# Optimization experiments

Measured on AMD Instinct MI355X. Metric: run time of the kernel, lower is better.

## Reference

```python
import jax, jax.numpy as jnp
import numpy as np

D_MODEL = 2048
N_HEADS = 16
HEAD_DIM = D_MODEL // N_HEADS  # 128
B, T = 2, 2048


def setup_inputs() -> dict:
    key = jax.random.key(0)
    ks = jax.random.split(key, 9)
    s = 0.02
    x = jax.random.normal(ks[0], (B, T, D_MODEL), dtype=jnp.float32)
    # Per-head projection weights (stacked over heads); torch Linear y = x @ W^T + b,
    # here W is stored as [H, d_model, head_dim] so y = einsum('btc,hcd->bhtd').
    Wq = jax.random.normal(ks[1], (N_HEADS, D_MODEL, HEAD_DIM), dtype=jnp.float32) * s
    bq = jax.random.normal(ks[2], (N_HEADS, HEAD_DIM), dtype=jnp.float32) * s
    Wk = jax.random.normal(ks[3], (N_HEADS, D_MODEL, HEAD_DIM), dtype=jnp.float32) * s
    bk = jax.random.normal(ks[4], (N_HEADS, HEAD_DIM), dtype=jnp.float32) * s
    Wv = jax.random.normal(ks[5], (N_HEADS, D_MODEL, HEAD_DIM), dtype=jnp.float32) * s
    bv = jax.random.normal(ks[6], (N_HEADS, HEAD_DIM), dtype=jnp.float32) * s
    Wo = jax.random.normal(ks[7], (D_MODEL, D_MODEL), dtype=jnp.float32) * s  # used as y @ Wo
    bo = jax.random.normal(ks[8], (D_MODEL,), dtype=jnp.float32) * s
    return {"x": x, "Wq": Wq, "bq": bq, "Wk": Wk, "bk": bk,
            "Wv": Wv, "bv": bv, "Wo": Wo, "bo": bo}


def reference(x, Wq, bq, Wk, bk, Wv, bv, Wo, bo):
    # x: [B, T, C]; per-head Q/K/V projections -> [B, H, T, D]
    Bn, Tn, C = x.shape
    H, _, D = Wq.shape
    scale = D ** (-0.5)
    q = jnp.einsum('btc,hcd->bhtd', x, Wq) + bq[None, :, None, :]
    k = jnp.einsum('btc,hcd->bhtd', x, Wk) + bk[None, :, None, :]
    v = jnp.einsum('btc,hcd->bhtd', x, Wv) + bv[None, :, None, :]
    # scores [B, H, T, T] with additive causal mask (finfo.min above the diagonal)
    scores = jnp.einsum('bhtd,bhsd->bhts', q, k) * scale
    neg = jnp.finfo(scores.dtype).min
    causal = jnp.triu(jnp.full((Tn, Tn), neg, dtype=scores.dtype), k=1)
    probs = jax.nn.softmax(scores + causal, axis=-1)
    y = jnp.einsum('bhts,bhsd->bhtd', probs, v)  # [B, H, T, D]
    # concat heads along feature dim (head order preserved) then output projection
    y = y.transpose(0, 2, 1, 3).reshape(Bn, Tn, H * D)
    return y @ Wo + bo
```

## Files before the change

kernel.cpp:

```cpp
#include <hip/hip_runtime.h>
#include <stdint.h>

typedef unsigned short u16;
typedef __attribute__((ext_vector_type(4))) u16 u16x4;
typedef __attribute__((ext_vector_type(8))) u16 u16x8;
typedef __attribute__((ext_vector_type(8))) __bf16 bf16x8;
typedef __attribute__((ext_vector_type(4))) float f32x4;

#define D_MODEL 2048
#define N_HEADS 16
#define HEAD_DIM 128
#define BATCH 2
#define SEQ 2048
#define M_TOT (BATCH*SEQ)
#define N_QKV (3*D_MODEL)

__device__ __forceinline__ u16 f2b(float f) {
  union { float f; uint32_t u; } c; c.f = f;
  uint32_t u = c.u;
  uint32_t r = (u + 0x7fffu + ((u >> 16) & 1u)) >> 16;
  return (u16)r;
}

__device__ __forceinline__ void gl_lds16(const u16* g, u16* l) {
  __builtin_amdgcn_global_load_lds(
      (const __attribute__((address_space(1))) uint32_t*)g,
      (__attribute__((address_space(3))) uint32_t*)l, 16, 0, 0);
}


__global__ void cast_x_kernel(const float* __restrict__ x, u16* __restrict__ xb, int n) {
  int i = (blockIdx.x * blockDim.x + threadIdx.x) * 4;
  if (i >= n) return;
  f32x4 v = *(const f32x4*)(x + i);
  u16x4 o;
  o[0] = f2b(v[0]); o[1] = f2b(v[1]); o[2] = f2b(v[2]); o[3] = f2b(v[3]);
  *(u16x4*)(xb + i) = o;
}

__global__ void trans_wqkv_kernel(const float* __restrict__ Wq, const float* __restrict__ Wk,
                                  const float* __restrict__ Wv, u16* __restrict__ Wt) {
  __shared__ u16 Tl[128][72];
  const int hh = blockIdx.y;
  const int qkv = hh >> 4, h = hh & 15;
  const float* src = (qkv == 0 ? Wq : qkv == 1 ? Wk : Wv) + (size_t)h * 2048 * 128;
  const int k0 = blockIdx.x * 64;
  const int tid = threadIdx.x;
  for (int it = 0; it < 32; ++it) {
    int idx = it * 256 + tid;
    int k = idx >> 7, d = idx & 127;
    Tl[d][k] = f2b(src[(size_t)(k0 + k) * 128 + d]);
  }
  __syncthreads();
  for (int it = 0; it < 32; ++it) {
    int idx = it * 256 + tid;
    int d = idx >> 6, kk = idx & 63;
    Wt[(size_t)(hh * 128 + d) * 2048 + k0 + kk] = Tl[d][kk];
  }
}

__global__ void trans_wo_kernel(const float* __restrict__ Wo, u16* __restrict__ Wot) {
  __shared__ u16 Tl[128][72];
  const int k0 = blockIdx.x * 64;
  const int n0 = blockIdx.y * 128;
  const int tid = threadIdx.x;
  for (int it = 0; it < 32; ++it) {
    int idx = it * 256 + tid;
    int k = idx >> 7, n = idx & 127;
    Tl[n][k] = f2b(Wo[(size_t)(k0 + k) * 2048 + n0 + n]);
  }
  __syncthreads();
  for (int it = 0; it < 32; ++it) {
    int idx = it * 256 + tid;
    int d = idx >> 6, kk = idx & 63;
    Wot[(size_t)(n0 + d) * 2048 + k0 + kk] = Tl[d][kk];
  }
}

__global__ void transpose_v_kernel(const u16* __restrict__ vb, u16* __restrict__ vt) {
  __shared__ u16 Tl[128 * 65];
  const int bh = blockIdx.y;
  const int t0 = blockIdx.x * 64;
  const int tid = threadIdx.x;
  const u16* src = vb + (size_t)bh * 2048 * 128;
  u16* dstp = vt + (size_t)bh * 128 * 2048;
#pragma unroll
  for (int c = 0; c < 4; ++c) {
    int ci = c * 256 + tid;
    int tr = ci >> 4, d0 = (ci & 15) * 8;
    u16x8 v = *(const u16x8*)(src + (size_t)(t0 + tr) * 128 + d0);
#pragma unroll
    for (int e = 0; e < 8; ++e) Tl[(d0 + e) * 65 + tr] = v[e];
  }
  __syncthreads();
#pragma unroll
  for (int it = 0; it < 32; ++it) {
    int idx = it * 256 + tid;
    int d = idx >> 6, tt = idx & 63;
    dstp[(size_t)d * 2048 + t0 + ((tt & 15) * 4 + (tt >> 4))] = Tl[d * 65 + tt];
  }
}

template <int EPI>
__global__ __launch_bounds__(256) void gemm_kernel(
    const u16* __restrict__ A, const u16* __restrict__ B,
    u16* __restrict__ qo, u16* __restrict__ ko, u16* __restrict__ vo,
    const float* __restrict__ bq, const float* __restrict__ bk, const float* __restrict__ bv,
    float* __restrict__ outf, const float* __restrict__ bo) {
  __shared__ u16 As[128 * 32];
  __shared__ u16 Bs[128 * 32];
  constexpr int NX = (EPI == 0) ? 48 : 16;
  const int nwg = gridDim.x;
  const int q8 = nwg >> 3;
  const int bid0 = blockIdx.x;
  const int gid = (bid0 & 7) * q8 + (bid0 >> 3);
  const int m0 = (gid / NX) * 128, n0 = (gid % NX) * 128;

  const int tid = threadIdx.x;
  const int lane = tid & 63, wv = tid >> 6;
  const int wm = (wv >> 1) * 64, wn = (wv & 1) * 64;
  const int lr = lane & 15, lk = (lane >> 4) * 8;

  f32x4 zero = {0.f, 0.f, 0.f, 0.f};
  f32x4 acc[4][4];
#pragma unroll
  for (int i = 0; i < 4; ++i)
#pragma unroll
    for (int j = 0; j < 4; ++j) acc[i][j] = zero;

  const int e0 = tid * 8;
  const int row0 = e0 >> 5;
  const int col0 = e0 & 31;
  const u16* Ag = A + (size_t)(m0 + row0) * 2048 + col0;
  const u16* Bg = B + (size_t)(n0 + row0) * 2048 + col0;

  for (int kt = 0; kt < 2048; kt += 32) {
    gl_lds16(Ag + kt, As + e0);
    gl_lds16(Ag + kt + (size_t)64 * 2048, As + e0 + 64 * 32);
    gl_lds16(Bg + kt, Bs + e0);
    gl_lds16(Bg + kt + (size_t)64 * 2048, Bs + e0 + 64 * 32);
    __syncthreads();
    bf16x8 af[4], bfm[4];
#pragma unroll
    for (int i = 0; i < 4; ++i) af[i] = *(const bf16x8*)(As + (wm + i * 16 + lr) * 32 + lk);
#pragma unroll
    for (int j = 0; j < 4; ++j) bfm[j] = *(const bf16x8*)(Bs + (wn + j * 16 + lr) * 32 + lk);
#pragma unroll
    for (int i = 0; i < 4; ++i)
#pragma unroll
      for (int j = 0; j < 4; ++j)
        acc[i][j] = __builtin_amdgcn_mfma_f32_16x16x32_bf16(af[i], bfm[j], acc[i][j], 0, 0, 0);
    __syncthreads();
  }

  const int rbase = (lane >> 4) * 4;
  if (EPI == 0) {
    const int qkv = n0 >> 11, h = (n0 >> 7) & 15;
    const float* bias = (qkv == 0) ? bq : (qkv == 1) ? bk : bv;
    u16* dst = (qkv == 0) ? qo : (qkv == 1) ? ko : vo;
    const float qscale = 0.08838834764831845f * 1.4426950408889634f;
#pragma unroll
    for (int i = 0; i < 4; ++i)
#pragma unroll
      for (int j = 0; j < 4; ++j)
#pragma unroll
        for (int r = 0; r < 4; ++r) {
          int gm = m0 + wm + i * 16 + rbase + r;
          int d = wn + j * 16 + (lane & 15);
          float val = acc[i][j][r] + bias[h * 128 + d];
          if (qkv == 0) val *= qscale;
          int b = gm >> 11, t = gm & 2047;
          dst[((size_t)(b * 16 + h) * 2048 + t) * 128 + d] = f2b(val);
        }
  } else {
#pragma unroll
    for (int i = 0; i < 4; ++i)
#pragma unroll
      for (int j = 0; j < 4; ++j)
#pragma unroll
        for (int r = 0; r < 4; ++r) {
          int gm = m0 + wm + i * 16 + rbase + r;
          int gn = n0 + wn + j * 16 + (lane & 15);
          outf[(size_t)gm * 2048 + gn] = acc[i][j][r] + bo[gn];
        }
  }
}

__global__ __launch_bounds__(256) void attn_kernel(
    const u16* __restrict__ qg, const u16* __restrict__ kg,
    const u16* __restrict__ vtg, u16* __restrict__ y) {
  __shared__ u16 Kb[2][64 * 128];
  __shared__ u16 Vb[2][128 * 64];
  __shared__ u16 Pl[4][32 * 64];
  const int tid = threadIdx.x, lane = tid & 63, w = tid >> 6;
  const int bid = blockIdx.x;
  const int bh = bid & 31, qt = 15 - (bid >> 5);
  const int b = bh >> 4, h = bh & 15;
  const int lr = lane & 15, lk = (lane >> 4) * 8;
  const u16* Qp = qg + (size_t)bh * (2048 * 128);
  const u16* Kp = kg + (size_t)bh * (2048 * 128);
  const u16* Vp = vtg + (size_t)bh * (128 * 2048);

  int koff[4], voff[4], dstc[4];
#pragma unroll
  for (int c = 0; c < 4; ++c) {
    int ci = c * 256 + tid;
    dstc[c] = ci * 8;
    int kr = ci >> 4, kj = ci & 15;
    koff[c] = kr * 128 + (kj ^ (kr & 7)) * 8;
    int vd = ci >> 3, vj = ci & 7;
    voff[c] = vd * 2048 + (vj ^ (vd & 7)) * 8;
  }
  const int kxor = (lr & 7) << 4;
  const int rbase = (lane >> 4) * 4;
  const f32x4 zero = {0.f, 0.f, 0.f, 0.f};

  const int q0 = qt * 128;
  const int qw = q0 + w * 32;
  const int nt = 2 * qt + 2;

  bf16x8 qf[2][4];
#pragma unroll
  for (int s = 0; s < 2; ++s)
#pragma unroll
    for (int i = 0; i < 4; ++i)
      qf[s][i] = *(const bf16x8*)(Qp + (size_t)(qw + s * 16 + lr) * 128 + i * 32 + lk);

  f32x4 o[2][8];
#pragma unroll
  for (int s = 0; s < 2; ++s)
#pragma unroll
    for (int f = 0; f < 8; ++f) o[s][f] = zero;
  float mrow[2][4], lrow[2][4];
#pragma unroll
  for (int s = 0; s < 2; ++s)
#pragma unroll
    for (int r = 0; r < 4; ++r) { mrow[s][r] = -1e30f; lrow[s][r] = 0.f; }

#pragma unroll
  for (int c = 0; c < 4; ++c) gl_lds16(Kp + koff[c], Kb[0] + dstc[c]);
#pragma unroll
  for (int c = 0; c < 4; ++c) gl_lds16(Vp + voff[c], Vb[0] + dstc[c]);
  __syncthreads();

  int cur = 0;
  for (int t = 0; t < nt; ++t) {
    const int s0 = t * 64;
    if (t + 1 < nt) {
      const size_t skn = (size_t)(s0 + 64) * 128;
#pragma unroll
      for (int c = 0; c < 4; ++c) gl_lds16(Kp + skn + koff[c], Kb[cur ^ 1] + dstc[c]);
#pragma unroll
      for (int c = 0; c < 4; ++c) gl_lds16(Vp + (s0 + 64) + voff[c], Vb[cur ^ 1] + dstc[c]);
    }
    if (s0 <= qw + 31) {
      const char* Kc = (const char*)Kb[cur];
      f32x4 sf[2][4];
      __builtin_amdgcn_s_setprio(1);
#pragma unroll
      for (int sj = 0; sj < 4; ++sj) {
        f32x4 a0 = zero, a1 = zero;
#pragma unroll
        for (int i = 0; i < 4; ++i) {
          bf16x8 kf = *(const bf16x8*)(Kc + ((((sj * 16 + lr) * 256) + (i * 32 + lk) * 2) ^ kxor));
          a0 = __builtin_amdgcn_mfma_f32_16x16x32_bf16(qf[0][i], kf, a0, 0, 0, 0);
          a1 = __builtin_amdgcn_mfma_f32_16x16x32_bf16(qf[1][i], kf, a1, 0, 0, 0);
        }
        sf[0][sj] = a0; sf[1][sj] = a1;
      }
      __builtin_amdgcn_s_setprio(0);

      char* Pc = (char*)Pl[w];
      const bool diag = (s0 + 63 > qw);
      float pmax[2][4];
      bool need = false;
#pragma unroll
      for (int s = 0; s < 2; ++s)
#pragma unroll
        for (int r = 0; r < 4; ++r) {
          if (diag) {
            const int rq = qw + s * 16 + rbase + r;
#pragma unroll
            for (int sj = 0; sj < 4; ++sj)
              if (s0 + sj * 16 + lr > rq) sf[s][sj][r] = -1e30f;
          }
          float pm = fmaxf(fmaxf(sf[s][0][r], sf[s][1][r]),
                           fmaxf(sf[s][2][r], sf[s][3][r]));
          pmax[s][r] = pm;
          need |= (pm > mrow[s][r] + 8.f);
        }
      if (__any(need)) {
#pragma unroll
        for (int s = 0; s < 2; ++s)
#pragma unroll
          for (int r = 0; r < 4; ++r) {
            float pm = pmax[s][r];
            pm = fmaxf(pm, __shfl_xor(pm, 1));
            pm = fmaxf(pm, __shfl_xor(pm, 2));
            pm = fmaxf(pm, __shfl_xor(pm, 4));
            pm = fmaxf(pm, __shfl_xor(pm, 8));
            float mnew = fmaxf(mrow[s][r], pm);
            float sfac = __builtin_amdgcn_exp2f(mrow[s][r] - mnew);
            mrow[s][r] = mnew;
            lrow[s][r] *= sfac;
#pragma unroll
            for (int f = 0; f < 8; ++f) o[s][f][r] *= sfac;
          }
      }
#pragma unroll
      for (int s = 0; s < 2; ++s)
#pragma unroll
        for (int r = 0; r < 4; ++r) {
          const int prow = s * 16 + rbase + r;
          u16x4 pk;
          float ps = 0.f;
#pragma unroll
          for (int sj = 0; sj < 4; ++sj) {
            float p = __builtin_amdgcn_exp2f(sf[s][sj][r] - mrow[s][r]);
            ps += p;
            pk[sj] = f2b(p);
          }
          lrow[s][r] += ps;
          *(u16x4*)(Pc + ((prow * 128 + lr * 8) ^ ((prow & 7) << 4))) = pk;
        }

      const char* Vc = (const char*)Vb[cur];
      __builtin_amdgcn_s_setprio(1);
#pragma unroll
      for (int st = 0; st < 2; ++st) {
        bf16x8 pf0 = *(const bf16x8*)(Pc + (((lr * 128) + (st * 32 + lk) * 2) ^ kxor));
        bf16x8 pf1 = *(const bf16x8*)(Pc + ((((16 + lr) * 128) + (st * 32 + lk) * 2) ^ kxor));
#pragma unroll
        for (int f = 0; f < 8; ++f) {
          bf16x8 vf = *(const bf16x8*)(Vc + ((((f * 16 + lr) * 128) + (st * 32 + lk) * 2) ^ kxor));
          o[0][f] = __builtin_amdgcn_mfma_f32_16x16x32_bf16(pf0, vf, o[0][f], 0, 0, 0);
          o[1][f] = __builtin_amdgcn_mfma_f32_16x16x32_bf16(pf1, vf, o[1][f], 0, 0, 0);
        }
      }
      __builtin_amdgcn_s_setprio(0);
    }
    __syncthreads();
    cur ^= 1;
  }

#pragma unroll
  for (int s = 0; s < 2; ++s)
#pragma unroll
    for (int r = 0; r < 4; ++r) {
      float l = lrow[s][r];
      l += __shfl_xor(l, 1);
      l += __shfl_xor(l, 2);
      l += __shfl_xor(l, 4);
      l += __shfl_xor(l, 8);
      const float rinv = __builtin_amdgcn_rcpf(l);
      const int row = qw + s * 16 + rbase + r;
#pragma unroll
      for (int f = 0; f < 8; ++f)
        y[((size_t)b * 2048 + row) * 2048 + h * 128 + f * 16 + lr] =
            f2b(o[s][f][r] * rinv);
    }
}


extern "C" void kernel_launch(void* const* d_in, const int* in_sizes, int n_in,
                              void* d_out, int out_size, void* d_ws, size_t ws_size,
                              hipStream_t stream) {
  const float* x  = (const float*)d_in[0];
  const float* Wq = (const float*)d_in[1];
  const float* bq = (const float*)d_in[2];
  const float* Wk = (const float*)d_in[3];
  const float* bk = (const float*)d_in[4];
  const float* Wv = (const float*)d_in[5];
  const float* bv = (const float*)d_in[6];
  const float* Wo = (const float*)d_in[7];
  const float* bo = (const float*)d_in[8];
  float* out = (float*)d_out;
  char* ws = (char*)d_ws;

  u16* xb  = (u16*)(ws + 0);
  u16* Wt  = (u16*)(ws + 16777216);
  u16* qb  = (u16*)(ws + 41943040);
  u16* kb  = (u16*)(ws + 58720256);
  u16* vb  = (u16*)(ws + 75497472);
  u16* Wot = Wt;
  u16* vtb = (u16*)(ws + 25165824);
  u16* yb  = xb;

  cast_x_kernel<<<8192, 256, 0, stream>>>(x, xb, M_TOT * D_MODEL);
  trans_wqkv_kernel<<<dim3(32, 48), 256, 0, stream>>>(Wq, Wk, Wv, Wt);
  gemm_kernel<0><<<N_QKV / 128 * (M_TOT / 128), 256, 0, stream>>>(
      xb, Wt, qb, kb, vb, bq, bk, bv, nullptr, nullptr);
  trans_wo_kernel<<<dim3(32, 16), 256, 0, stream>>>(Wo, Wot);
  transpose_v_kernel<<<dim3(32, 32), 256, 0, stream>>>(vb, vtb);
  attn_kernel<<<512, 256, 0, stream>>>(qb, kb, vtb, yb);
  gemm_kernel<1><<<D_MODEL / 128 * (M_TOT / 128), 256, 0, stream>>>(
      yb, Wot, nullptr, nullptr, nullptr, nullptr, nullptr, nullptr, out, bo);
}
```

Measured before the change: 306.5 us.

## Rewrite projection GEMMs with larger tiles, triple-buffered LDS pipeline and swizzling

Replaces the generic 128x128 GEMM with two specialized kernels. Each uses 512-thread blocks with 256x384 (QKV) or 256x128 (output) tiles, a three-stage global-to-LDS prefetch pipeline synchronized through vmcnt waits and raw barriers, and XOR-swizzled LDS layouts to avoid bank conflicts. The QKV GEMM also switches to 32x32x16 MFMA. Each grid has 256 blocks, matching the CU count, and blocks are remapped for L2 locality. The aim is to hide load latency behind MFMA work and raise arithmetic intensity, at the cost of higher register and LDS pressure and hand-tuned wait counts that are easy to get wrong.

```diff
diff --git a/kernel.cpp b/kernel.cpp
--- a/kernel.cpp
+++ b/kernel.cpp
@@ -6,6 +6,7 @@
 typedef __attribute__((ext_vector_type(8))) u16 u16x8;
 typedef __attribute__((ext_vector_type(8))) __bf16 bf16x8;
 typedef __attribute__((ext_vector_type(4))) float f32x4;
+typedef __attribute__((ext_vector_type(16))) float f32x16;
 
 #define D_MODEL 2048
 #define N_HEADS 16
@@ -26,6 +27,12 @@
   __builtin_amdgcn_global_load_lds(
       (const __attribute__((address_space(1))) uint32_t*)g,
       (__attribute__((address_space(3))) uint32_t*)l, 16, 0, 0);
+}
+
+template <int N> __device__ __forceinline__ void waitvm() {
+  if constexpr (N == 6)      asm volatile("s_waitcnt vmcnt(6)" ::: "memory");
+  else if constexpr (N == 5) asm volatile("s_waitcnt vmcnt(5)" ::: "memory");
+  else                       asm volatile("s_waitcnt vmcnt(0)" ::: "memory");
 }
 
 
@@ -101,88 +108,206 @@
   }
 }
 
-template <int EPI>
-__global__ __launch_bounds__(256) void gemm_kernel(
+__global__ __launch_bounds__(512, 2) void gemm_qkv_kernel(
     const u16* __restrict__ A, const u16* __restrict__ B,
     u16* __restrict__ qo, u16* __restrict__ ko, u16* __restrict__ vo,
-    const float* __restrict__ bq, const float* __restrict__ bk, const float* __restrict__ bv,
-    float* __restrict__ outf, const float* __restrict__ bo) {
-  __shared__ u16 As[128 * 32];
-  __shared__ u16 Bs[128 * 32];
-  constexpr int NX = (EPI == 0) ? 48 : 16;
-  const int nwg = gridDim.x;
-  const int q8 = nwg >> 3;
+    const float* __restrict__ bq, const float* __restrict__ bk, const float* __restrict__ bv) {
+  __shared__ u16 LS[3][20480];
   const int bid0 = blockIdx.x;
-  const int gid = (bid0 & 7) * q8 + (bid0 >> 3);
-  const int m0 = (gid / NX) * 128, n0 = (gid % NX) * 128;
-
-  const int tid = threadIdx.x;
-  const int lane = tid & 63, wv = tid >> 6;
-  const int wm = (wv >> 1) * 64, wn = (wv & 1) * 64;
-  const int lr = lane & 15, lk = (lane >> 4) * 8;
-
-  f32x4 zero = {0.f, 0.f, 0.f, 0.f};
-  f32x4 acc[4][4];
-#pragma unroll
-  for (int i = 0; i < 4; ++i)
-#pragma unroll
-    for (int j = 0; j < 4; ++j) acc[i][j] = zero;
-
-  const int e0 = tid * 8;
-  const int row0 = e0 >> 5;
-  const int col0 = e0 & 31;
-  const u16* Ag = A + (size_t)(m0 + row0) * 2048 + col0;
-  const u16* Bg = B + (size_t)(n0 + row0) * 2048 + col0;
-
-  for (int kt = 0; kt < 2048; kt += 32) {
-    gl_lds16(Ag + kt, As + e0);
-    gl_lds16(Ag + kt + (size_t)64 * 2048, As + e0 + 64 * 32);
-    gl_lds16(Bg + kt, Bs + e0);
-    gl_lds16(Bg + kt + (size_t)64 * 2048, Bs + e0 + 64 * 32);
-    __syncthreads();
-    bf16x8 af[4], bfm[4];
-#pragma unroll
-    for (int i = 0; i < 4; ++i) af[i] = *(const bf16x8*)(As + (wm + i * 16 + lr) * 32 + lk);
-#pragma unroll
-    for (int j = 0; j < 4; ++j) bfm[j] = *(const bf16x8*)(Bs + (wn + j * 16 + lr) * 32 + lk);
-#pragma unroll
-    for (int i = 0; i < 4; ++i)
-#pragma unroll
-      for (int j = 0; j < 4; ++j)
-        acc[i][j] = __builtin_amdgcn_mfma_f32_16x16x32_bf16(af[i], bfm[j], acc[i][j], 0, 0, 0);
-    __syncthreads();
-  }
-
-  const int rbase = (lane >> 4) * 4;
-  if (EPI == 0) {
-    const int qkv = n0 >> 11, h = (n0 >> 7) & 15;
+  const int gid = (bid0 & 7) * 32 + (bid0 >> 3);
+  const int G = gid >> 4, l = gid & 15;
+  const int m0 = ((G & 3) * 4 + (l & 3)) * 256;
+  const int n0 = ((G >> 2) * 4 + (l >> 2)) * 384;
+
+  const int tid = threadIdx.x, lane = tid & 63, w = tid >> 6;
+  const int wm = (w >> 2) * 128, wn = (w & 3) * 96;
+  const int l31 = lane & 31, g2 = lane >> 5;
+  const int kx = ((l31 >> 1) & 3) << 4;
+
+  int aoff[2], boff[3];
+#pragma unroll
+  for (int l2 = 0; l2 < 2; ++l2) {
+    int ci = l2 * 512 + tid, r = ci >> 2, j = ci & 3;
+    aoff[l2] = (m0 + r) * 2048 + (j ^ ((r >> 1) & 3)) * 8;
+  }
+#pragma unroll
+  for (int l2 = 0; l2 < 3; ++l2) {
+    int ci = l2 * 512 + tid, r = ci >> 2, j = ci & 3;
+    boff[l2] = (n0 + r) * 2048 + (j ^ ((r >> 1) & 3)) * 8;
+  }
+  const int adl = tid * 8;
+  const int bdl = 8192 + tid * 8;
+
+  f32x16 acc[4][3];
+#pragma unroll
+  for (int ai = 0; ai < 4; ++ai)
+#pragma unroll
+    for (int bj = 0; bj < 3; ++bj)
+#pragma unroll
+      for (int e = 0; e < 16; ++e) acc[ai][bj][e] = 0.f;
+
+#pragma unroll
+  for (int t = 0; t < 2; ++t) {
+#pragma unroll
+    for (int l2 = 0; l2 < 2; ++l2) gl_lds16(A + aoff[l2] + t * 32, LS[t] + adl + l2 * 4096);
+#pragma unroll
+    for (int l2 = 0; l2 < 3; ++l2) gl_lds16(B + boff[l2] + t * 32, LS[t] + bdl + l2 * 4096);
+  }
+  waitvm<5>();
+  __builtin_amdgcn_s_barrier();
+
+  int s = 0;
+  for (int kt = 0; kt < 64; ++kt) {
+    if (kt < 62) {
+      const int s2 = (s == 0) ? 2 : s - 1;
+      const int k2 = (kt + 2) * 32;
+#pragma unroll
+      for (int l2 = 0; l2 < 2; ++l2) gl_lds16(A + aoff[l2] + k2, LS[s2] + adl + l2 * 4096);
+#pragma unroll
+      for (int l2 = 0; l2 < 3; ++l2) gl_lds16(B + boff[l2] + k2, LS[s2] + bdl + l2 * 4096);
+    }
+    const char* base = (const char*)LS[s];
+#pragma unroll
+    for (int kk = 0; kk < 2; ++kk) {
+      bf16x8 af[4];
+#pragma unroll
+      for (int ai = 0; ai < 4; ++ai) {
+        int r = wm + ai * 32 + l31;
+        af[ai] = *(const bf16x8*)(base + r * 64 + ((32 * kk + 16 * g2) ^ kx));
+      }
+      __builtin_amdgcn_s_setprio(1);
+#pragma unroll
+      for (int bj = 0; bj < 3; ++bj) {
+        int rb = wn + bj * 32 + l31;
+        bf16x8 bfr = *(const bf16x8*)(base + 16384 + rb * 64 + ((32 * kk + 16 * g2) ^ kx));
+#pragma unroll
+        for (int ai = 0; ai < 4; ++ai)
+          acc[ai][bj] = __builtin_amdgcn_mfma_f32_32x32x16_bf16(af[ai], bfr, acc[ai][bj], 0, 0, 0);
+      }
+      __builtin_amdgcn_s_setprio(0);
+    }
+    if (kt < 62)       waitvm<5>();
+    else if (kt == 62) waitvm<0>();
+    __builtin_amdgcn_s_barrier();
+    s = (s == 2) ? 0 : s + 1;
+  }
+
+  const float qscale = 0.08838834764831845f * 1.4426950408889634f;
+#pragma unroll
+  for (int bj = 0; bj < 3; ++bj) {
+    const int n = n0 + wn + bj * 32 + l31;
+    const int qkv = n >> 11, hh = (n >> 7) & 15, d = n & 127;
     const float* bias = (qkv == 0) ? bq : (qkv == 1) ? bk : bv;
     u16* dst = (qkv == 0) ? qo : (qkv == 1) ? ko : vo;
-    const float qscale = 0.08838834764831845f * 1.4426950408889634f;
-#pragma unroll
-    for (int i = 0; i < 4; ++i)
-#pragma unroll
-      for (int j = 0; j < 4; ++j)
-#pragma unroll
-        for (int r = 0; r < 4; ++r) {
-          int gm = m0 + wm + i * 16 + rbase + r;
-          int d = wn + j * 16 + (lane & 15);
-          float val = acc[i][j][r] + bias[h * 128 + d];
-          if (qkv == 0) val *= qscale;
-          int b = gm >> 11, t = gm & 2047;
-          dst[((size_t)(b * 16 + h) * 2048 + t) * 128 + d] = f2b(val);
-        }
-  } else {
-#pragma unroll
-    for (int i = 0; i < 4; ++i)
-#pragma unroll
-      for (int j = 0; j < 4; ++j)
-#pragma unroll
-        for (int r = 0; r < 4; ++r) {
-          int gm = m0 + wm + i * 16 + rbase + r;
-          int gn = n0 + wn + j * 16 + (lane & 15);
-          outf[(size_t)gm * 2048 + gn] = acc[i][j][r] + bo[gn];
-        }
+    const float bv_ = bias[n & 2047];
+#pragma unroll
+    for (int ai = 0; ai < 4; ++ai)
+#pragma unroll
+      for (int e = 0; e < 16; ++e) {
+        int row = (e & 3) + 8 * (e >> 2) + 4 * g2;
+        int gm = m0 + wm + ai * 32 + row;
+        float val = acc[ai][bj][e] + bv_;
+        if (qkv == 0) val *= qscale;
+        int b = gm >> 11, t = gm & 2047;
+        dst[((size_t)(b * 16 + hh) * 2048 + t) * 128 + d] = f2b(val);
+      }
+  }
+}
+
+__global__ __launch_bounds__(512, 2) void gemm_out_kernel(
+    const u16* __restrict__ A, const u16* __restrict__ B,
+    float* __restrict__ outf, const float* __restrict__ bo) {
+  __shared__ u16 LS[3][24576];
+  const int bid0 = blockIdx.x;
+  const int gid = (bid0 & 7) * 32 + (bid0 >> 3);
+  const int G = gid >> 4, l = gid & 15;
+  const int m0 = ((G & 3) * 4 + (l & 3)) * 256;
+  const int n0 = ((G >> 2) * 4 + (l >> 2)) * 128;
+
+  const int tid = threadIdx.x, lane = tid & 63, w = tid >> 6;
+  const int wm = (w >> 1) * 64, wn = (w & 1) * 64;
+  const int lr = lane & 15, g = lane >> 4;
+  const int kx = (lr & 7) << 4;
+
+  int aoff[4], boff[2];
+#pragma unroll
+  for (int l2 = 0; l2 < 4; ++l2) {
+    int ci = l2 * 512 + tid, r = ci >> 3, gj = ci & 7;
+    aoff[l2] = (m0 + r) * 2048 + (gj ^ (r & 7)) * 8;
+  }
+#pragma unroll
+  for (int l2 = 0; l2 < 2; ++l2) {
+    int ci = l2 * 512 + tid, r = ci >> 3, gj = ci & 7;
+    boff[l2] = (n0 + r) * 2048 + (gj ^ (r & 7)) * 8;
+  }
+  const int adl = tid * 8;
+  const int bdl = 16384 + tid * 8;
+
+  f32x4 acc[4][4];
+  const f32x4 zero = {0.f, 0.f, 0.f, 0.f};
+#pragma unroll
+  for (int ai = 0; ai < 4; ++ai)
+#pragma unroll
+    for (int bj = 0; bj < 4; ++bj) acc[ai][bj] = zero;
+
+#pragma unroll
+  for (int t = 0; t < 2; ++t) {
+#pragma unroll
+    for (int l2 = 0; l2 < 4; ++l2) gl_lds16(A + aoff[l2] + t * 64, LS[t] + adl + l2 * 4096);
+#pragma unroll
+    for (int l2 = 0; l2 < 2; ++l2) gl_lds16(B + boff[l2] + t * 64, LS[t] + bdl + l2 * 4096);
+  }
+  waitvm<6>();
+  __builtin_amdgcn_s_barrier();
+
+  int s = 0;
+  for (int kt = 0; kt < 32; ++kt) {
+    if (kt < 30) {
+      const int s2 = (s == 0) ? 2 : s - 1;
+      const int k2 = (kt + 2) * 64;
+#pragma unroll
+      for (int l2 = 0; l2 < 4; ++l2) gl_lds16(A + aoff[l2] + k2, LS[s2] + adl + l2 * 4096);
+#pragma unroll
+      for (int l2 = 0; l2 < 2; ++l2) gl_lds16(B + boff[l2] + k2, LS[s2] + bdl + l2 * 4096);
+    }
+    const char* base = (const char*)LS[s];
+#pragma unroll
+    for (int h = 0; h < 2; ++h) {
+      bf16x8 af[4];
+#pragma unroll
+      for (int ai = 0; ai < 4; ++ai) {
+        int r = wm + ai * 16 + lr;
+        af[ai] = *(const bf16x8*)(base + r * 128 + ((h * 64 + 16 * g) ^ kx));
+      }
+      __builtin_amdgcn_s_setprio(1);
+#pragma unroll
+      for (int bj = 0; bj < 4; ++bj) {
+        int rb = wn + bj * 16 + lr;
+        bf16x8 bfr = *(const bf16x8*)(base + 32768 + rb * 128 + ((h * 64 + 16 * g) ^ kx));
+#pragma unroll
+        for (int ai = 0; ai < 4; ++ai)
+          acc[ai][bj] = __builtin_amdgcn_mfma_f32_16x16x32_bf16(af[ai], bfr, acc[ai][bj], 0, 0, 0);
+      }
+      __builtin_amdgcn_s_setprio(0);
+    }
+    if (kt < 30)       waitvm<6>();
+    else if (kt == 30) waitvm<0>();
+    __builtin_amdgcn_s_barrier();
+    s = (s == 2) ? 0 : s + 1;
+  }
+
+  const int rbase = g * 4;
+#pragma unroll
+  for (int bj = 0; bj < 4; ++bj) {
+    const int gn = n0 + wn + bj * 16 + lr;
+    const float bv_ = bo[gn];
+#pragma unroll
+    for (int ai = 0; ai < 4; ++ai)
+#pragma unroll
+      for (int r = 0; r < 4; ++r) {
+        int gm = m0 + wm + ai * 16 + rbase + r;
+        outf[(size_t)gm * 2048 + gn] = acc[ai][bj][r] + bv_;
+      }
   }
 }
 
@@ -388,11 +513,9 @@
 
   cast_x_kernel<<<8192, 256, 0, stream>>>(x, xb, M_TOT * D_MODEL);
   trans_wqkv_kernel<<<dim3(32, 48), 256, 0, stream>>>(Wq, Wk, Wv, Wt);
-  gemm_kernel<0><<<N_QKV / 128 * (M_TOT / 128), 256, 0, stream>>>(
-      xb, Wt, qb, kb, vb, bq, bk, bv, nullptr, nullptr);
+  gemm_qkv_kernel<<<256, 512, 0, stream>>>(xb, Wt, qb, kb, vb, bq, bk, bv);
   trans_wo_kernel<<<dim3(32, 16), 256, 0, stream>>>(Wo, Wot);
   transpose_v_kernel<<<dim3(32, 32), 256, 0, stream>>>(vb, vtb);
   attn_kernel<<<512, 256, 0, stream>>>(qb, kb, vtb, yb);
-  gemm_kernel<1><<<D_MODEL / 128 * (M_TOT / 128), 256, 0, stream>>>(
-      yb, Wot, nullptr, nullptr, nullptr, nullptr, nullptr, nullptr, out, bo);
-}
+  gemm_out_kernel<<<256, 512, 0, stream>>>(yb, Wot, out, bo);
+}
```

After: 282.9 us. -7.7%, faster.
